# Optimization experiments

Hardware: AMD Instinct MI355X
Metric: run time of the kernel (lower is better)

## Reference

```python
import jax, jax.numpy as jnp
import numpy as np

TOPK = 6
E = 512
IN = 384
M = 8192
LN_EPS = 1e-5


def _lin(x, w, b):
    # torch nn.Linear: y = x @ W^T + b, W is [out, in]
    return x @ w.T + b


def setup_inputs() -> dict:
    key = jax.random.key(0)
    ks = jax.random.split(key, 16)
    s = lambda k, sh: (jax.random.normal(k, sh, dtype=jnp.float32) * 0.02)
    return {
        "x": jax.random.normal(ks[0], (1, M, IN), dtype=jnp.float32),
        "fc1_w": s(ks[1], (E, IN)), "fc1_b": jnp.zeros((E,), jnp.float32),
        "wh_w": s(ks[2], (E, E)),   "wh_b": jnp.zeros((E,), jnp.float32),
        "wt_w": s(ks[3], (E, E)),   "wt_b": jnp.zeros((E,), jnp.float32),
        "l1_w": s(ks[4], (E, E)),   "l1_b": jnp.zeros((E,), jnp.float32),
        "l2_w": s(ks[5], (E, E)),   "l2_b": jnp.zeros((E,), jnp.float32),
        "a1_w": s(ks[6], (E // 2, E)), "a1_b": jnp.zeros((E // 2,), jnp.float32),
        "a2_w": s(ks[7], (1, E // 2)), "a2_b": jnp.zeros((1,), jnp.float32),
        "ln_g": jnp.ones((E,), jnp.float32), "ln_b": jnp.zeros((E,), jnp.float32),
    }


def reference(x, fc1_w, fc1_b, wh_w, wh_b, wt_w, wt_b,
              l1_w, l1_b, l2_w, l2_b, a1_w, a1_b, a2_w, a2_b, ln_g, ln_b):
    lrelu = jax.nn.leaky_relu  # slope 0.01 == torch default
    h = lrelu(_lin(x, fc1_w, fc1_b))                      # [B,M,E]
    h = (h + h.mean(axis=1, keepdims=True)) * 0.5
    e_h = _lin(h, wh_w, wh_b)                             # [B,M,E]
    e_t = _lin(h, wt_w, wt_b)                             # [B,M,E]
    scale = E ** (-0.5)
    attn_logit = (e_h * scale) @ jnp.swapaxes(e_t, -2, -1)  # [B,M,M]
    topk_weight, topk_index = jax.lax.top_k(attn_logit, TOPK)  # [B,M,K]
    # gather top-k neighbor tail embeddings: [B,M,K,E]
    Nb_h = jax.vmap(lambda et, idx: et[idx])(e_t, topk_index)
    topk_prob = jax.nn.softmax(topk_weight, axis=2)       # [B,M,K]
    eh_r = topk_prob[..., None] * Nb_h + (1.0 - topk_prob)[..., None] * e_h[:, :, None, :]
    gate = jnp.tanh(e_h[:, :, None, :] + eh_r)            # [B,M,K,E]
    # faithful to torch einsum('ijkl,ijkm->ijk'): sums l and m independently
    ka_weight = Nb_h.sum(axis=-1) * gate.sum(axis=-1)     # [B,M,K]
    ka_prob = jax.nn.softmax(ka_weight, axis=2)           # [B,M,K]
    e_Nh = jnp.einsum('bmk,bmke->bme', ka_prob, Nb_h)     # [B,M,E]
    sum_emb = lrelu(_lin(e_h + e_Nh, l1_w, l1_b))
    bi_emb = lrelu(_lin(e_h * e_Nh, l2_w, l2_b))
    emb = sum_emb + bi_emb                                # [B,M,E] (dropout = eval identity)
    hn = emb[0]                                           # squeeze(0) -> [M,E]
    # GeoGlobalAttention readout: gate_nn = Linear->LeakyReLU->Linear, softmax over nodes
    g = _lin(lrelu(_lin(hn, a1_w, a1_b)), a2_w, a2_b)     # [M,1]
    att = jax.nn.softmax(g, axis=0)
    pooled = (att * hn).sum(axis=0, keepdims=True)        # [1,E]
    mu = pooled.mean(axis=-1, keepdims=True)
    var = jnp.mean((pooled - mu) ** 2, axis=-1, keepdims=True)
    out = (pooled - mu) / jnp.sqrt(var + LN_EPS) * ln_g + ln_b
    return out
```

## Files before the change

kernel.cpp:

```cpp
#include <hip/hip_runtime.h>
#include <math.h>
#include <stdint.h>

#define M_NODES 8192
#define E_DIM   512
#define NTOPK   6
#define ATTN_SCALE 0.04419417382415922f
#define NEG_BIG (-1e38f)
#define CAND_CAP 192

typedef __attribute__((ext_vector_type(8))) short short8;
typedef __attribute__((ext_vector_type(4))) float f32x4;

__device__ __forceinline__ float lrelu(float v) { return v > 0.f ? v : 0.01f * v; }

__device__ __forceinline__ unsigned short f2bf(float f) {
  uint32_t u = __float_as_uint(f);
  uint32_t r = (u + 0x7FFFu + ((u >> 16) & 1u)) >> 16;
  return (unsigned short)r;
}
__device__ __forceinline__ float bf2f(unsigned short s) {
  return __uint_as_float(((uint32_t)s) << 16);
}

__device__ __forceinline__ void async_cp16(const void* gptr, void* lds) {
  auto g1 = reinterpret_cast<const __attribute__((address_space(1))) unsigned int*>(
      reinterpret_cast<uintptr_t>(gptr));
  auto l3 = reinterpret_cast<__attribute__((address_space(3))) unsigned int*>(
      reinterpret_cast<uintptr_t>(lds));
  __builtin_amdgcn_global_load_lds(g1, l3, 16, 0, 0);
}



__global__ __launch_bounds__(256) void wcast_kernel(
    const float* __restrict__ x, const float* __restrict__ fc1w,
    const float* __restrict__ whw, const float* __restrict__ wtw,
    const float* __restrict__ l1w, const float* __restrict__ l2w,
    const float* __restrict__ a1w,
    unsigned short* __restrict__ xT, unsigned short* __restrict__ fc1T,
    unsigned short* __restrict__ whT, unsigned short* __restrict__ wtT,
    unsigned short* __restrict__ l1T, unsigned short* __restrict__ l2T,
    unsigned short* __restrict__ a1T)
{
  const int gid = blockIdx.x * 256 + threadIdx.x;
  const float* src; unsigned short* dst; int K8, local;
  if (gid < 417792) {
    K8 = 48;
    if (gid < 393216) { src = x; dst = xT; local = gid; }
    else { src = fc1w; dst = fc1T; local = gid - 393216; }
  } else {
    K8 = 64;
    if (gid < 450560)      { src = whw; dst = whT; local = gid - 417792; }
    else if (gid < 483328) { src = wtw; dst = wtT; local = gid - 450560; }
    else if (gid < 516096) { src = l1w; dst = l1T; local = gid - 483328; }
    else if (gid < 548864) { src = l2w; dst = l2T; local = gid - 516096; }
    else                   { src = a1w; dst = a1T; local = gid - 548864; }
  }
  const int m = local / K8;
  const int k8 = local - m * K8;
  const float* p = src + (size_t)m * (K8 * 8) + k8 * 8;
  float4 v0 = ((const float4*)p)[0];
  float4 v1 = ((const float4*)p)[1];
  const int Kt = K8 >> 2;
  const size_t ti = ((size_t)(m >> 4) * Kt + (k8 >> 2)) * 512 + ((m & 15) + 16 * (k8 & 3)) * 8;
  uint4 pk;
  pk.x = (uint32_t)f2bf(v0.x) | ((uint32_t)f2bf(v0.y) << 16);
  pk.y = (uint32_t)f2bf(v0.z) | ((uint32_t)f2bf(v0.w) << 16);
  pk.z = (uint32_t)f2bf(v1.x) | ((uint32_t)f2bf(v1.y) << 16);
  pk.w = (uint32_t)f2bf(v1.z) | ((uint32_t)f2bf(v1.w) << 16);
  *(uint4*)(dst + ti) = pk;
}

template <int MODE>
__global__ __launch_bounds__(256) void mfma_gemm(
    const unsigned short* __restrict__ At1, const unsigned short* __restrict__ At2,
    const unsigned short* __restrict__ Wt1, const unsigned short* __restrict__ Wt2,
    const float* __restrict__ b1, const float* __restrict__ b2,
    float* __restrict__ Cf, unsigned short* __restrict__ T1,
    unsigned short* __restrict__ T2, unsigned short* __restrict__ Cbf,
    unsigned short* __restrict__ Cbf2, int N, int K)
{
  constexpr bool DUALW = (MODE == 1 || MODE == 2);
  __shared__ unsigned short As[2][8 * 512];
  __shared__ unsigned short Bs[2][4 * 512];
  const int Kt = K >> 5;
  const int tid = threadIdx.x, lane = tid & 63, w = tid >> 6;
  const int m0 = blockIdx.y * 128, n0 = blockIdx.x * 64;

  f32x4 acc0[2][4], acc1[2][4];
#pragma unroll
  for (int p = 0; p < 2; p++)
#pragma unroll
    for (int j = 0; j < 4; j++) {
      acc0[p][j] = (f32x4){0.f, 0.f, 0.f, 0.f};
      acc1[p][j] = (f32x4){0.f, 0.f, 0.f, 0.f};
    }

  for (int kt = 0; kt < Kt; kt++) {
    const unsigned short* a1p = At1 + ((size_t)((m0 >> 4) + 2 * w) * Kt + kt) * 512 + lane * 8;
    async_cp16(a1p, &As[0][(2 * w) * 512]);
    async_cp16(a1p + (size_t)Kt * 512, &As[0][(2 * w + 1) * 512]);
    if (MODE == 2) {
      const unsigned short* a2p = At2 + ((size_t)((m0 >> 4) + 2 * w) * Kt + kt) * 512 + lane * 8;
      async_cp16(a2p, &As[1][(2 * w) * 512]);
      async_cp16(a2p + (size_t)Kt * 512, &As[1][(2 * w + 1) * 512]);
    }
    const unsigned short* bp1 = Wt1 + ((size_t)((n0 >> 4) + w) * Kt + kt) * 512 + lane * 8;
    async_cp16(bp1, &Bs[0][w * 512]);
    if (DUALW) {
      const unsigned short* bp2 = Wt2 + ((size_t)((n0 >> 4) + w) * Kt + kt) * 512 + lane * 8;
      async_cp16(bp2, &Bs[1][w * 512]);
    }
    __syncthreads();
    short8 a[2], a2[2], bb[4], bb2[4];
#pragma unroll
    for (int p = 0; p < 2; p++) a[p] = *(const short8*)&As[0][(2 * w + p) * 512 + lane * 8];
    if (MODE == 2) {
#pragma unroll
      for (int p = 0; p < 2; p++) a2[p] = *(const short8*)&As[1][(2 * w + p) * 512 + lane * 8];
    }
#pragma unroll
    for (int j = 0; j < 4; j++) bb[j] = *(const short8*)&Bs[0][j * 512 + lane * 8];
    if (DUALW) {
#pragma unroll
      for (int j = 0; j < 4; j++) bb2[j] = *(const short8*)&Bs[1][j * 512 + lane * 8];
    }
#pragma unroll
    for (int p = 0; p < 2; p++)
#pragma unroll
      for (int j = 0; j < 4; j++) {
        acc0[p][j] = __builtin_amdgcn_mfma_f32_16x16x32_bf16(a[p], bb[j], acc0[p][j], 0, 0, 0);
        if (MODE == 1)
          acc1[p][j] = __builtin_amdgcn_mfma_f32_16x16x32_bf16(a[p], bb2[j], acc1[p][j], 0, 0, 0);
        if (MODE == 2)
          acc1[p][j] = __builtin_amdgcn_mfma_f32_16x16x32_bf16(a2[p], bb2[j], acc1[p][j], 0, 0, 0);
      }
    __syncthreads();
  }

  const int lrow = (lane >> 4) * 4, lcol = lane & 15;

  if (MODE == 3) {
    float part[2][4] = {};
#pragma unroll
    for (int p = 0; p < 2; p++)
#pragma unroll
      for (int j = 0; j < 4; j++) {
        const int c = n0 + j * 16 + lcol;
        const float bias1 = b1[c];
        const float w2 = b2[c];
#pragma unroll
        for (int d = 0; d < 4; d++)
          part[p][d] = fmaf(lrelu(acc0[p][j][d] + bias1), w2, part[p][d]);
      }
#pragma unroll
    for (int p = 0; p < 2; p++)
#pragma unroll
      for (int d = 0; d < 4; d++) {
#pragma unroll
        for (int off = 1; off < 16; off <<= 1)
          part[p][d] += __shfl_xor(part[p][d], off);
      }
    if (lcol == 0) {
#pragma unroll
      for (int p = 0; p < 2; p++)
#pragma unroll
        for (int d = 0; d < 4; d++)
          atomicAdd(&Cf[m0 + w * 32 + p * 16 + lrow + d], part[p][d]);
    }
    return;
  }

  const int NT = N >> 5;
#pragma unroll
  for (int p = 0; p < 2; p++)
#pragma unroll
    for (int j = 0; j < 4; j++) {
      const int c = n0 + j * 16 + lcol;
      const float bias1 = b1[c];
      const float bias2 = DUALW ? b2[c] : 0.f;
#pragma unroll
      for (int d = 0; d < 4; d++) {
        const int r = m0 + w * 32 + p * 16 + lrow + d;
        const float v0 = acc0[p][j][d] + bias1;
        if (MODE == 0) {
          Cf[(size_t)r * N + c] = lrelu(v0);
        } else {
          const size_t ti = ((size_t)(r >> 4) * NT + (c >> 5)) * 512 +
                            ((r & 15) + 16 * ((c >> 3) & 3)) * 8 + (c & 7);
          if (MODE == 1) {
            const float v1 = acc1[p][j][d] + bias2;
            T1[ti] = f2bf(v0);
            T2[ti] = f2bf(v1);
            Cbf[(size_t)r * N + c] = f2bf(v0);
            Cbf2[(size_t)r * N + c] = f2bf(v1);
          } else {
            const float e = lrelu(v0) + lrelu(acc1[p][j][d] + bias2);
            T1[ti] = f2bf(e);
            Cbf[(size_t)r * N + c] = f2bf(e);
          }
        }
      }
    }
}

__global__ __launch_bounds__(256) void colsum_kernel(const float* __restrict__ h,
                                                     float* __restrict__ colsum)
{
  const int t = threadIdx.x;
  const int r0 = blockIdx.x * 128;
  float s0 = 0.f, s1 = 0.f;
  for (int r = 0; r < 128; r++) {
    s0 += h[(size_t)(r0 + r) * E_DIM + t];
    s1 += h[(size_t)(r0 + r) * E_DIM + 256 + t];
  }
  atomicAdd(&colsum[t], s0);
  atomicAdd(&colsum[t + 256], s1);
}

__global__ __launch_bounds__(256) void hupd_cast_kernel(
    const float* __restrict__ h, const float* __restrict__ colsum,
    unsigned short* __restrict__ hT)
{
  const int gid = blockIdx.x * 256 + threadIdx.x;
  const int m = gid >> 6, k8 = gid & 63;
  const float* p = h + (size_t)m * E_DIM + k8 * 8;
  float4 v0 = ((const float4*)p)[0];
  float4 v1 = ((const float4*)p)[1];
  float4 c0 = *(const float4*)(colsum + k8 * 8);
  float4 c1 = *(const float4*)(colsum + k8 * 8 + 4);
  const float im = 1.f / (float)M_NODES;
  v0.x = (v0.x + c0.x * im) * 0.5f; v0.y = (v0.y + c0.y * im) * 0.5f;
  v0.z = (v0.z + c0.z * im) * 0.5f; v0.w = (v0.w + c0.w * im) * 0.5f;
  v1.x = (v1.x + c1.x * im) * 0.5f; v1.y = (v1.y + c1.y * im) * 0.5f;
  v1.z = (v1.z + c1.z * im) * 0.5f; v1.w = (v1.w + c1.w * im) * 0.5f;
  const size_t ti = ((size_t)(m >> 4) * 16 + (k8 >> 2)) * 512 + ((m & 15) + 16 * (k8 & 3)) * 8;
  uint4 pk;
  pk.x = (uint32_t)f2bf(v0.x) | ((uint32_t)f2bf(v0.y) << 16);
  pk.y = (uint32_t)f2bf(v0.z) | ((uint32_t)f2bf(v0.w) << 16);
  pk.z = (uint32_t)f2bf(v1.x) | ((uint32_t)f2bf(v1.y) << 16);
  pk.w = (uint32_t)f2bf(v1.z) | ((uint32_t)f2bf(v1.w) << 16);
  *(uint4*)(hT + ti) = pk;
}

__global__ __launch_bounds__(256, 4) void sgemm_kernel(
    const unsigned short* __restrict__ ehT, const unsigned short* __restrict__ etT,
    unsigned short* __restrict__ sc, float* __restrict__ tmax)
{
  __shared__ unsigned short As[8 * 512];
  __shared__ unsigned short Bs[8 * 512];
  const int tid = threadIdx.x, lane = tid & 63, w = tid >> 6;
  const int wr = w >> 1, wc = w & 1;
  const int m0 = blockIdx.y * 128;
  const int n0 = blockIdx.x * 128;

  f32x4 acc[4][4];
#pragma unroll
  for (int i = 0; i < 4; i++)
#pragma unroll
    for (int j = 0; j < 4; j++) acc[i][j] = (f32x4){0.f, 0.f, 0.f, 0.f};

  for (int kt = 0; kt < 16; kt++) {
    const int s0 = w, s1 = w + 4;
    async_cp16(ehT + ((size_t)((m0 >> 4) + s0) * 16 + kt) * 512 + lane * 8, &As[s0 * 512]);
    async_cp16(ehT + ((size_t)((m0 >> 4) + s1) * 16 + kt) * 512 + lane * 8, &As[s1 * 512]);
    async_cp16(etT + ((size_t)((n0 >> 4) + s0) * 16 + kt) * 512 + lane * 8, &Bs[s0 * 512]);
    async_cp16(etT + ((size_t)((n0 >> 4) + s1) * 16 + kt) * 512 + lane * 8, &Bs[s1 * 512]);
    __syncthreads();
    short8 a[4], b[4];
#pragma unroll
    for (int i = 0; i < 4; i++) a[i] = *(const short8*)&As[(wr * 4 + i) * 512 + lane * 8];
#pragma unroll
    for (int j = 0; j < 4; j++) b[j] = *(const short8*)&Bs[(wc * 4 + j) * 512 + lane * 8];
#pragma unroll
    for (int i = 0; i < 4; i++)
#pragma unroll
      for (int j = 0; j < 4; j++)
        acc[i][j] = __builtin_amdgcn_mfma_f32_16x16x32_bf16(a[i], b[j], acc[i][j], 0, 0, 0);
    __syncthreads();
  }

  const int q = lane >> 4, lcol = lane & 15;
  const size_t blkbase = ((size_t)blockIdx.y * 64 + blockIdx.x) * 16384;

  float rm[4][4];
#pragma unroll
  for (int i = 0; i < 4; i++)
#pragma unroll
    for (int d = 0; d < 4; d++) rm[i][d] = NEG_BIG;

#pragma unroll
  for (int i = 0; i < 4; i++)
#pragma unroll
    for (int jj = 0; jj < 2; jj++) {
      unsigned short o[8];
#pragma unroll
      for (int d = 0; d < 4; d++) {
        o[d] = f2bf(acc[i][2 * jj][d]);
        o[4 + d] = f2bf(acc[i][2 * jj + 1][d]);
        rm[i][d] = fmaxf(rm[i][d], fmaxf(bf2f(o[d]), bf2f(o[4 + d])));
      }
      const size_t off = blkbase + (size_t)(wr * 4 + i) * 2048 + q * 512 +
                         (wc * 32 + jj * 16 + lcol) * 8;
      *(short8*)(sc + off) = *(short8*)o;
    }

#pragma unroll
  for (int i = 0; i < 4; i++)
#pragma unroll
    for (int d = 0; d < 4; d++) {
#pragma unroll
      for (int off = 1; off < 16; off <<= 1)
        rm[i][d] = fmaxf(rm[i][d], __shfl_xor(rm[i][d], off));
    }

  if (lcol == 0) {
#pragma unroll
    for (int i = 0; i < 4; i++)
#pragma unroll
      for (int d = 0; d < 4; d++)
        tmax[(size_t)(m0 + wr * 64 + i * 16 + q * 4 + d) * 128 +
             blockIdx.x * 2 + wc] = rm[i][d];
  }
}

__global__ __launch_bounds__(256) void scan_topk_kernel(
    const unsigned short* __restrict__ sc, const float* __restrict__ tmax,
    float* __restrict__ tkv, int* __restrict__ tki)
{
  __shared__ float cv[4][CAND_CAP];
  __shared__ int   ci[4][CAND_CAP];
  __shared__ int   cnt[4];
  __shared__ float taus[4];
  const int tid = threadIdx.x;
  const int lane = tid & 63;
  const int w = tid >> 6;
  const int rg = blockIdx.x;
  const int bm = rg >> 5;
  const int g = rg & 31;
  const int wr = g >> 4, gi = (g >> 2) & 3, gq = g & 3;
  const int r0 = bm * 128 + wr * 64 + gi * 16 + gq * 4;

  if (tid < 4) cnt[tid] = 0;

  {
    const float* tm = tmax + (size_t)(r0 + w) * 128;
    const float v2 = fmaxf(tm[lane], tm[lane + 64]);
    uint32_t u = __float_as_uint(v2);
    u = ((int)u >= 0) ? (u | 0x80000000u) : ~u;
    uint32_t key = (u & ~63u) | (uint32_t)lane;
    float tau = 0.f;
#pragma unroll
    for (int it = 0; it < 6; it++) {
      uint32_t k = key;
#pragma unroll
      for (int off = 32; off; off >>= 1) {
        const uint32_t o = (uint32_t)__shfl_xor((int)k, off);
        k = k > o ? k : o;
      }
      const int wl = (int)(k & 63u);
      if (it == 5) tau = __shfl(v2, wl);
      if (lane == wl) key = 0u;
    }
    if (lane == 0) taus[w] = tau;
  }
  __syncthreads();
  const float t0 = taus[0], t1 = taus[1], t2 = taus[2], t3 = taus[3];

  const size_t rowoff = (size_t)(wr * 4 + gi) * 2048 + gq * 512 + lane * 8;
  const int colbase = (lane >> 5) * 64 + 2 * ((lane >> 4) & 1) * 16 + (lane & 15);
  for (int t = 0; t < 16; t++) {
    const int bn = w * 16 + t;
    short8 u = *(const short8*)(sc + ((size_t)(bm * 64 + bn)) * 16384 + rowoff);
    const int cb = bn * 128 + colbase;
#pragma unroll
    for (int e = 0; e < 8; e++) {
      const float f = bf2f((unsigned short)u[e]);
      const int d = e & 3;
      const float tau = (d == 0) ? t0 : (d == 1) ? t1 : (d == 2) ? t2 : t3;
      if (f >= tau) {
        const int slot = atomicAdd(&cnt[d], 1);
        if (slot < CAND_CAP) {
          cv[d][slot] = f;
          ci[d][slot] = cb + (e >> 2) * 16;
        }
      }
    }
  }
  __syncthreads();

  int n = cnt[w];
  n = n < CAND_CAP ? n : CAND_CAP;
  for (int c = lane; c < n; c += 64) {
    const float v = cv[w][c];
    const int idx = ci[w][c];
    int rank = 0;
    for (int j = 0; j < n; j++) {
      const float vj = cv[w][j];
      rank += (vj > v) || (vj == v && ci[w][j] < idx);
    }
    if (rank < NTOPK) {
      const size_t base = (size_t)(r0 + w) * NTOPK + rank;
      tkv[base] = v * ATTN_SCALE;
      tki[base] = idx;
    }
  }
}

__global__ __launch_bounds__(256) void combine_kernel(
    const unsigned short* __restrict__ ehRow, const unsigned short* __restrict__ etRow,
    const float* __restrict__ tkv, const int* __restrict__ tki,
    unsigned short* __restrict__ s1T, unsigned short* __restrict__ s2T)
{
  const int lane = threadIdx.x & 63;
  const int m = blockIdx.x * 4 + (threadIdx.x >> 6);

  float wv[NTOPK]; int id[NTOPK];
#pragma unroll
  for (int k = 0; k < NTOPK; k++) {
    wv[k] = tkv[(size_t)m * NTOPK + k];
    id[k] = tki[(size_t)m * NTOPK + k];
  }

  float mx = wv[0];
#pragma unroll
  for (int k = 1; k < NTOPK; k++) mx = fmaxf(mx, wv[k]);
  float p[NTOPK]; float s = 0.f;
#pragma unroll
  for (int k = 0; k < NTOPK; k++) { p[k] = expf(wv[k] - mx); s += p[k]; }
  const float inv = 1.f / s;
#pragma unroll
  for (int k = 0; k < NTOPK; k++) p[k] *= inv;

  short8 eh8 = *(const short8*)(ehRow + (size_t)m * E_DIM + lane * 8);
  float ehv[8];
#pragma unroll
  for (int e = 0; e < 8; e++) ehv[e] = bf2f((unsigned short)eh8[e]);

  float nv[NTOPK][8];
#pragma unroll
  for (int k = 0; k < NTOPK; k++) {
    short8 nb = *(const short8*)(etRow + (size_t)id[k] * E_DIM + lane * 8);
#pragma unroll
    for (int e = 0; e < 8; e++) nv[k][e] = bf2f((unsigned short)nb[e]);
  }

  float ka[NTOPK];
#pragma unroll
  for (int k = 0; k < NTOPK; k++) {
    float snb = 0.f, sg = 0.f;
    const float aa = 2.f - p[k], bb = p[k];
#pragma unroll
    for (int e = 0; e < 8; e++) {
      snb += nv[k][e];
      sg += tanhf(fmaf(aa, ehv[e], bb * nv[k][e]));
    }
#pragma unroll
    for (int off = 32; off; off >>= 1) {
      snb += __shfl_xor(snb, off);
      sg += __shfl_xor(sg, off);
    }
    ka[k] = snb * sg;
  }
  float km = ka[0];
#pragma unroll
  for (int k = 1; k < NTOPK; k++) km = fmaxf(km, ka[k]);
  float kp[NTOPK]; float ks = 0.f;
#pragma unroll
  for (int k = 0; k < NTOPK; k++) { kp[k] = expf(ka[k] - km); ks += kp[k]; }
  const float kinv = 1.f / ks;

  const size_t tbase = ((size_t)(m >> 4) * 16 + (lane >> 2)) * 512 +
                       ((m & 15) + 16 * (lane & 3)) * 8;
  unsigned short o1[8], o2[8];
#pragma unroll
  for (int e = 0; e < 8; e++) {
    float o = 0.f;
#pragma unroll
    for (int k = 0; k < NTOPK; k++) o = fmaf(kp[k], nv[k][e], o);
    o *= kinv;
    o1[e] = f2bf(ehv[e] + o);
    o2[e] = f2bf(ehv[e] * o);
  }
  *(short8*)(s1T + tbase) = *(short8*)o1;
  *(short8*)(s2T + tbase) = *(short8*)o2;
}

__global__ __launch_bounds__(1024) void softmax_stats_kernel(
    const float* __restrict__ g, float* __restrict__ stats)
{
  __shared__ float red[16];
  __shared__ float red2[16];
  const int t = threadIdx.x;
  float mx = NEG_BIG;
  for (int i = t; i < M_NODES; i += 1024) mx = fmaxf(mx, g[i]);
#pragma unroll
  for (int off = 32; off; off >>= 1) mx = fmaxf(mx, __shfl_xor(mx, off));
  if ((t & 63) == 0) red[t >> 6] = mx;
  __syncthreads();
  float gmx = red[0];
  for (int i = 1; i < 16; i++) gmx = fmaxf(gmx, red[i]);
  float s = 0.f;
  for (int i = t; i < M_NODES; i += 1024) s += expf(g[i] - gmx);
#pragma unroll
  for (int off = 32; off; off >>= 1) s += __shfl_xor(s, off);
  if ((t & 63) == 0) red2[t >> 6] = s;
  __syncthreads();
  if (t == 0) {
    float tot = 0.f;
    for (int i = 0; i < 16; i++) tot += red2[i];
    stats[0] = gmx; stats[1] = tot;
  }
}

__global__ __launch_bounds__(256) void pooled_kernel(
    const unsigned short* __restrict__ emb, const float* __restrict__ g,
    const float* __restrict__ stats, float* __restrict__ pooled)
{
  const int t = threadIdx.x;
  const int r0 = blockIdx.x * 128;
  const float mx = stats[0];
  const float inv = 1.f / stats[1];
  float a0 = 0.f, a1 = 0.f;
  for (int r = 0; r < 128; r++) {
    const int m = r0 + r;
    const float wv = expf(g[m] - mx) * inv;
    a0 = fmaf(wv, bf2f(emb[(size_t)m * E_DIM + t]), a0);
    a1 = fmaf(wv, bf2f(emb[(size_t)m * E_DIM + 256 + t]), a1);
  }
  atomicAdd(&pooled[t], a0);
  atomicAdd(&pooled[t + 256], a1);
}

__global__ __launch_bounds__(512) void ln_kernel(
    const float* __restrict__ pooled, const float* __restrict__ lng,
    const float* __restrict__ lnb, float* __restrict__ out)
{
  __shared__ float red[8];
  __shared__ float red2[8];
  const int t = threadIdx.x;
  const float v = pooled[t];
  float s = v;
#pragma unroll
  for (int off = 32; off; off >>= 1) s += __shfl_xor(s, off);
  if ((t & 63) == 0) red[t >> 6] = s;
  __syncthreads();
  float tot = 0.f;
  for (int i = 0; i < 8; i++) tot += red[i];
  const float mu = tot / (float)E_DIM;
  const float d = v - mu;
  float q = d * d;
#pragma unroll
  for (int off = 32; off; off >>= 1) q += __shfl_xor(q, off);
  if ((t & 63) == 0) red2[t >> 6] = q;
  __syncthreads();
  float vt = 0.f;
  for (int i = 0; i < 8; i++) vt += red2[i];
  const float var = vt / (float)E_DIM;
  out[t] = d * rsqrtf(var + 1e-5f) * lng[t] + lnb[t];
}

extern "C" void kernel_launch(void* const* d_in, const int* in_sizes, int n_in,
                              void* d_out, int out_size, void* d_ws, size_t ws_size,
                              hipStream_t stream)
{
  const float* x     = (const float*)d_in[0];
  const float* fc1_w = (const float*)d_in[1];
  const float* fc1_b = (const float*)d_in[2];
  const float* wh_w  = (const float*)d_in[3];
  const float* wh_b  = (const float*)d_in[4];
  const float* wt_w  = (const float*)d_in[5];
  const float* wt_b  = (const float*)d_in[6];
  const float* l1_w  = (const float*)d_in[7];
  const float* l1_b  = (const float*)d_in[8];
  const float* l2_w  = (const float*)d_in[9];
  const float* l2_b  = (const float*)d_in[10];
  const float* a1_w  = (const float*)d_in[11];
  const float* a1_b  = (const float*)d_in[12];
  const float* a2_w  = (const float*)d_in[13];
  const float* a2_b  = (const float*)d_in[14];
  const float* ln_g  = (const float*)d_in[15];
  const float* ln_b  = (const float*)d_in[16];
  (void)a2_b;

  char* ws = (char*)d_ws;
  const size_t MiB = 1 << 20;
  unsigned short* fc1T = (unsigned short*)(ws + 0);
  unsigned short* whT  = (unsigned short*)(ws + 393216);
  unsigned short* wtT  = (unsigned short*)(ws + 917504);
  unsigned short* l1T  = (unsigned short*)(ws + 1441792);
  unsigned short* l2T  = (unsigned short*)(ws + 1966080);
  unsigned short* a1T  = (unsigned short*)(ws + 2490368);
  unsigned short* xT     = (unsigned short*)(ws + 3 * MiB);
  float*          h      = (float*)(ws + 9 * MiB);
  unsigned short* hT     = (unsigned short*)(ws + 25 * MiB);
  unsigned short* ehT    = (unsigned short*)(ws + 33 * MiB);
  unsigned short* etT    = (unsigned short*)(ws + 41 * MiB);
  unsigned short* ehRow  = (unsigned short*)(ws + 49 * MiB);
  unsigned short* etRow  = (unsigned short*)(ws + 57 * MiB);
  float*          tmaxb  = (float*)(ws + 65 * MiB);
  unsigned short* s1T    = (unsigned short*)(ws + 3 * MiB);
  unsigned short* s2T    = (unsigned short*)(ws + 11 * MiB);
  unsigned short* embT   = (unsigned short*)(ws + 19 * MiB);
  unsigned short* embRow = (unsigned short*)(ws + 27 * MiB);
  unsigned short* scores = (unsigned short*)(ws + 96 * MiB);
  char*           smal   = ws + 69 * MiB;
  float* tkv    = (float*)(smal);
  int*   tki    = (int*)(smal + 196608);
  float* colsum = (float*)(smal + 393216);
  float* g      = (float*)(smal + 395264);
  float* stats  = (float*)(smal + 428032);
  float* pooled = (float*)(smal + 432128);

  hipMemsetAsync(smal, 0, 436224, stream);

  wcast_kernel<<<2208, 256, 0, stream>>>(x, fc1_w, wh_w, wt_w, l1_w, l2_w, a1_w,
                                         xT, fc1T, whT, wtT, l1T, l2T, a1T);
  mfma_gemm<0><<<dim3(8, 64), 256, 0, stream>>>(
      xT, nullptr, fc1T, nullptr, fc1_b, nullptr, h, nullptr, nullptr, nullptr, nullptr,
      512, 384);
  colsum_kernel<<<64, 256, 0, stream>>>(h, colsum);
  hupd_cast_kernel<<<2048, 256, 0, stream>>>(h, colsum, hT);
  mfma_gemm<1><<<dim3(8, 64), 256, 0, stream>>>(
      hT, nullptr, whT, wtT, wh_b, wt_b, nullptr, ehT, etT, ehRow, etRow, 512, 512);
  sgemm_kernel<<<dim3(64, 64), 256, 0, stream>>>(ehT, etT, scores, tmaxb);
  scan_topk_kernel<<<M_NODES / 4, 256, 0, stream>>>(scores, tmaxb, tkv, tki);
  combine_kernel<<<M_NODES / 4, 256, 0, stream>>>(ehRow, etRow, tkv, tki, s1T, s2T);
  mfma_gemm<2><<<dim3(8, 64), 256, 0, stream>>>(
      s1T, s2T, l1T, l2T, l1_b, l2_b, nullptr, embT, nullptr, embRow, nullptr, 512, 512);
  mfma_gemm<3><<<dim3(4, 64), 256, 0, stream>>>(
      embT, nullptr, a1T, nullptr, a1_b, a2_w, g, nullptr, nullptr, nullptr, nullptr,
      256, 512);
  softmax_stats_kernel<<<1, 1024, 0, stream>>>(g, stats);
  pooled_kernel<<<64, 256, 0, stream>>>(embRow, g, stats, pooled);
  ln_kernel<<<1, 512, 0, stream>>>(pooled, ln_g, ln_b, (float*)d_out);
}
```

Before: 323.0 us.

## Fuse colsum into fc1 GEMM, merge top-k scan with combine, drop softmax stats

The fc1 GEMM now writes bf16 rows and accumulates column sums with atomics, which removes the separate fp32 h buffer and the colsum pass. The score matrix is stored row-major per 128-column block, and the scan uses per-block maxima to skip blocks that cannot hold a top-6 candidate. The scan is fused with the combine kernel so top-k results stay in shared memory. The softmax-statistics kernel is dropped in favour of unnormalised exp weights plus an atomic sum that ln divides out. This risks overflow without max subtraction, and rounding h to bf16 before the mean changes precision.

```diff
diff --git a/kernel.cpp b/kernel.cpp
--- a/kernel.cpp
+++ b/kernel.cpp
@@ -172,6 +172,35 @@
     return;
   }
 
+  if (MODE == 4) {
+    float colp[4] = {};
+#pragma unroll
+    for (int p = 0; p < 2; p++)
+#pragma unroll
+      for (int j = 0; j < 4; j++) {
+        const int c = n0 + j * 16 + lcol;
+        const float bias1 = b1[c];
+#pragma unroll
+        for (int d = 0; d < 4; d++) {
+          const int r = m0 + w * 32 + p * 16 + lrow + d;
+          const float v = lrelu(acc0[p][j][d] + bias1);
+          Cbf[(size_t)r * N + c] = f2bf(v);
+          colp[j] += v;
+        }
+      }
+#pragma unroll
+    for (int j = 0; j < 4; j++) {
+      colp[j] += __shfl_xor(colp[j], 16);
+      colp[j] += __shfl_xor(colp[j], 32);
+    }
+    if (lane < 16) {
+#pragma unroll
+      for (int j = 0; j < 4; j++)
+        atomicAdd(&Cf[n0 + j * 16 + lcol], colp[j]);
+    }
+    return;
+  }
+
   const int NT = N >> 5;
 #pragma unroll
   for (int p = 0; p < 2; p++)
@@ -184,63 +213,46 @@
       for (int d = 0; d < 4; d++) {
         const int r = m0 + w * 32 + p * 16 + lrow + d;
         const float v0 = acc0[p][j][d] + bias1;
-        if (MODE == 0) {
-          Cf[(size_t)r * N + c] = lrelu(v0);
+        const size_t ti = ((size_t)(r >> 4) * NT + (c >> 5)) * 512 +
+                          ((r & 15) + 16 * ((c >> 3) & 3)) * 8 + (c & 7);
+        if (MODE == 1) {
+          const float v1 = acc1[p][j][d] + bias2;
+          T1[ti] = f2bf(v0);
+          T2[ti] = f2bf(v1);
+          Cbf[(size_t)r * N + c] = f2bf(v0);
+          Cbf2[(size_t)r * N + c] = f2bf(v1);
         } else {
-          const size_t ti = ((size_t)(r >> 4) * NT + (c >> 5)) * 512 +
-                            ((r & 15) + 16 * ((c >> 3) & 3)) * 8 + (c & 7);
-          if (MODE == 1) {
-            const float v1 = acc1[p][j][d] + bias2;
-            T1[ti] = f2bf(v0);
-            T2[ti] = f2bf(v1);
-            Cbf[(size_t)r * N + c] = f2bf(v0);
-            Cbf2[(size_t)r * N + c] = f2bf(v1);
-          } else {
-            const float e = lrelu(v0) + lrelu(acc1[p][j][d] + bias2);
-            T1[ti] = f2bf(e);
-            Cbf[(size_t)r * N + c] = f2bf(e);
-          }
+          const float e = lrelu(v0) + lrelu(acc1[p][j][d] + bias2);
+          T1[ti] = f2bf(e);
+          Cbf[(size_t)r * N + c] = f2bf(e);
         }
       }
     }
 }
 
-__global__ __launch_bounds__(256) void colsum_kernel(const float* __restrict__ h,
-                                                     float* __restrict__ colsum)
-{
-  const int t = threadIdx.x;
-  const int r0 = blockIdx.x * 128;
-  float s0 = 0.f, s1 = 0.f;
-  for (int r = 0; r < 128; r++) {
-    s0 += h[(size_t)(r0 + r) * E_DIM + t];
-    s1 += h[(size_t)(r0 + r) * E_DIM + 256 + t];
-  }
-  atomicAdd(&colsum[t], s0);
-  atomicAdd(&colsum[t + 256], s1);
-}
-
 __global__ __launch_bounds__(256) void hupd_cast_kernel(
-    const float* __restrict__ h, const float* __restrict__ colsum,
+    const unsigned short* __restrict__ hRow, const float* __restrict__ colsum,
     unsigned short* __restrict__ hT)
 {
   const int gid = blockIdx.x * 256 + threadIdx.x;
   const int m = gid >> 6, k8 = gid & 63;
-  const float* p = h + (size_t)m * E_DIM + k8 * 8;
-  float4 v0 = ((const float4*)p)[0];
-  float4 v1 = ((const float4*)p)[1];
+  short8 hv = *(const short8*)(hRow + (size_t)m * E_DIM + k8 * 8);
   float4 c0 = *(const float4*)(colsum + k8 * 8);
   float4 c1 = *(const float4*)(colsum + k8 * 8 + 4);
   const float im = 1.f / (float)M_NODES;
-  v0.x = (v0.x + c0.x * im) * 0.5f; v0.y = (v0.y + c0.y * im) * 0.5f;
-  v0.z = (v0.z + c0.z * im) * 0.5f; v0.w = (v0.w + c0.w * im) * 0.5f;
-  v1.x = (v1.x + c1.x * im) * 0.5f; v1.y = (v1.y + c1.y * im) * 0.5f;
-  v1.z = (v1.z + c1.z * im) * 0.5f; v1.w = (v1.w + c1.w * im) * 0.5f;
+  float v[8];
+#pragma unroll
+  for (int e = 0; e < 8; e++) v[e] = bf2f((unsigned short)hv[e]);
+  v[0] = (v[0] + c0.x * im) * 0.5f; v[1] = (v[1] + c0.y * im) * 0.5f;
+  v[2] = (v[2] + c0.z * im) * 0.5f; v[3] = (v[3] + c0.w * im) * 0.5f;
+  v[4] = (v[4] + c1.x * im) * 0.5f; v[5] = (v[5] + c1.y * im) * 0.5f;
+  v[6] = (v[6] + c1.z * im) * 0.5f; v[7] = (v[7] + c1.w * im) * 0.5f;
   const size_t ti = ((size_t)(m >> 4) * 16 + (k8 >> 2)) * 512 + ((m & 15) + 16 * (k8 & 3)) * 8;
   uint4 pk;
-  pk.x = (uint32_t)f2bf(v0.x) | ((uint32_t)f2bf(v0.y) << 16);
-  pk.y = (uint32_t)f2bf(v0.z) | ((uint32_t)f2bf(v0.w) << 16);
-  pk.z = (uint32_t)f2bf(v1.x) | ((uint32_t)f2bf(v1.y) << 16);
-  pk.w = (uint32_t)f2bf(v1.z) | ((uint32_t)f2bf(v1.w) << 16);
+  pk.x = (uint32_t)f2bf(v[0]) | ((uint32_t)f2bf(v[1]) << 16);
+  pk.y = (uint32_t)f2bf(v[2]) | ((uint32_t)f2bf(v[3]) << 16);
+  pk.z = (uint32_t)f2bf(v[4]) | ((uint32_t)f2bf(v[5]) << 16);
+  pk.w = (uint32_t)f2bf(v[6]) | ((uint32_t)f2bf(v[7]) << 16);
   *(uint4*)(hT + ti) = pk;
 }
 
@@ -282,7 +294,7 @@
   }
 
   const int q = lane >> 4, lcol = lane & 15;
-  const size_t blkbase = ((size_t)blockIdx.y * 64 + blockIdx.x) * 16384;
+  const int bn = blockIdx.x;
 
   float rm[4][4];
 #pragma unroll
@@ -293,17 +305,16 @@
 #pragma unroll
   for (int i = 0; i < 4; i++)
 #pragma unroll
-    for (int jj = 0; jj < 2; jj++) {
-      unsigned short o[8];
-#pragma unroll
-      for (int d = 0; d < 4; d++) {
-        o[d] = f2bf(acc[i][2 * jj][d]);
-        o[4 + d] = f2bf(acc[i][2 * jj + 1][d]);
-        rm[i][d] = fmaxf(rm[i][d], fmaxf(bf2f(o[d]), bf2f(o[4 + d])));
+    for (int d = 0; d < 4; d++) {
+      unsigned short o[4];
+#pragma unroll
+      for (int j = 0; j < 4; j++) {
+        o[j] = f2bf(acc[i][j][d]);
+        rm[i][d] = fmaxf(rm[i][d], bf2f(o[j]));
       }
-      const size_t off = blkbase + (size_t)(wr * 4 + i) * 2048 + q * 512 +
-                         (wc * 32 + jj * 16 + lcol) * 8;
-      *(short8*)(sc + off) = *(short8*)o;
+      const int row = m0 + wr * 64 + i * 16 + q * 4 + d;
+      const size_t off = ((size_t)row * 64 + bn) * 128 + (wc * 16 + lcol) * 4;
+      *(uint2*)(sc + off) = *(uint2*)o;
     }
 
 #pragma unroll
@@ -321,70 +332,65 @@
 #pragma unroll
       for (int d = 0; d < 4; d++)
         tmax[(size_t)(m0 + wr * 64 + i * 16 + q * 4 + d) * 128 +
-             blockIdx.x * 2 + wc] = rm[i][d];
-  }
-}
-
-__global__ __launch_bounds__(256) void scan_topk_kernel(
+             bn * 2 + wc] = rm[i][d];
+  }
+}
+
+__global__ __launch_bounds__(256) void scan_combine_kernel(
     const unsigned short* __restrict__ sc, const float* __restrict__ tmax,
-    float* __restrict__ tkv, int* __restrict__ tki)
+    const unsigned short* __restrict__ ehRow, const unsigned short* __restrict__ etRow,
+    unsigned short* __restrict__ s1T, unsigned short* __restrict__ s2T)
 {
   __shared__ float cv[4][CAND_CAP];
   __shared__ int   ci[4][CAND_CAP];
   __shared__ int   cnt[4];
-  __shared__ float taus[4];
+  __shared__ float t6v[4][8];
+  __shared__ int   t6i[4][8];
   const int tid = threadIdx.x;
   const int lane = tid & 63;
   const int w = tid >> 6;
-  const int rg = blockIdx.x;
-  const int bm = rg >> 5;
-  const int g = rg & 31;
-  const int wr = g >> 4, gi = (g >> 2) & 3, gq = g & 3;
-  const int r0 = bm * 128 + wr * 64 + gi * 16 + gq * 4;
-
-  if (tid < 4) cnt[tid] = 0;
-
-  {
-    const float* tm = tmax + (size_t)(r0 + w) * 128;
-    const float v2 = fmaxf(tm[lane], tm[lane + 64]);
-    uint32_t u = __float_as_uint(v2);
-    u = ((int)u >= 0) ? (u | 0x80000000u) : ~u;
-    uint32_t key = (u & ~63u) | (uint32_t)lane;
-    float tau = 0.f;
-#pragma unroll
-    for (int it = 0; it < 6; it++) {
-      uint32_t k = key;
-#pragma unroll
-      for (int off = 32; off; off >>= 1) {
-        const uint32_t o = (uint32_t)__shfl_xor((int)k, off);
-        k = k > o ? k : o;
-      }
-      const int wl = (int)(k & 63u);
-      if (it == 5) tau = __shfl(v2, wl);
-      if (lane == wl) key = 0u;
-    }
-    if (lane == 0) taus[w] = tau;
-  }
-  __syncthreads();
-  const float t0 = taus[0], t1 = taus[1], t2 = taus[2], t3 = taus[3];
-
-  const size_t rowoff = (size_t)(wr * 4 + gi) * 2048 + gq * 512 + lane * 8;
-  const int colbase = (lane >> 5) * 64 + 2 * ((lane >> 4) & 1) * 16 + (lane & 15);
-  for (int t = 0; t < 16; t++) {
-    const int bn = w * 16 + t;
-    short8 u = *(const short8*)(sc + ((size_t)(bm * 64 + bn)) * 16384 + rowoff);
-    const int cb = bn * 128 + colbase;
-#pragma unroll
-    for (int e = 0; e < 8; e++) {
-      const float f = bf2f((unsigned short)u[e]);
-      const int d = e & 3;
-      const float tau = (d == 0) ? t0 : (d == 1) ? t1 : (d == 2) ? t2 : t3;
+  const int row = blockIdx.x * 4 + w;
+
+  if (lane == 0) cnt[w] = 0;
+  if (lane < 8) { t6v[w][lane] = 0.f; t6i[w][lane] = 0; }
+
+  const float* tm = tmax + (size_t)row * 128;
+  const float v2 = fmaxf(tm[lane], tm[lane + 64]);
+  const float bmax = fmaxf(tm[2 * lane], tm[2 * lane + 1]);
+  uint32_t u = __float_as_uint(v2);
+  u = ((int)u >= 0) ? (u | 0x80000000u) : ~u;
+  uint32_t key = (u & ~63u) | (uint32_t)lane;
+  float tau = 0.f;
+#pragma unroll
+  for (int it = 0; it < 6; it++) {
+    uint32_t k = key;
+#pragma unroll
+    for (int off = 32; off; off >>= 1) {
+      const uint32_t o = (uint32_t)__shfl_xor((int)k, off);
+      k = k > o ? k : o;
+    }
+    const int wl = (int)(k & 63u);
+    if (it == 5) tau = __shfl(v2, wl);
+    if (lane == wl) key = 0u;
+  }
+
+  unsigned long long mask = __ballot(bmax >= tau);
+  const unsigned short* rp = sc + (size_t)row * 8192;
+  while (mask) {
+    const int bn = __ffsll(mask) - 1;
+    mask &= mask - 1;
+    const uint32_t uu = *(const uint32_t*)(rp + bn * 128 + lane * 2);
+    const float f0 = bf2f((unsigned short)(uu & 0xFFFFu));
+    const float f1 = bf2f((unsigned short)(uu >> 16));
+#pragma unroll
+    for (int e = 0; e < 2; e++) {
+      const float f = e ? f1 : f0;
       if (f >= tau) {
-        const int slot = atomicAdd(&cnt[d], 1);
-        if (slot < CAND_CAP) {
-          cv[d][slot] = f;
-          ci[d][slot] = cb + (e >> 2) * 16;
-        }
+        const int idx128 = lane * 2 + e;
+        const int g = idx128 >> 2, j = idx128 & 3;
+        const int col = bn * 128 + (g >> 4) * 64 + j * 16 + (g & 15);
+        const int slot = atomicAdd(&cnt[w], 1);
+        if (slot < CAND_CAP) { cv[w][slot] = f; ci[w][slot] = col; }
       }
     }
   }
@@ -400,27 +406,16 @@
       const float vj = cv[w][j];
       rank += (vj > v) || (vj == v && ci[w][j] < idx);
     }
-    if (rank < NTOPK) {
-      const size_t base = (size_t)(r0 + w) * NTOPK + rank;
-      tkv[base] = v * ATTN_SCALE;
-      tki[base] = idx;
-    }
-  }
-}
-
-__global__ __launch_bounds__(256) void combine_kernel(
-    const unsigned short* __restrict__ ehRow, const unsigned short* __restrict__ etRow,
-    const float* __restrict__ tkv, const int* __restrict__ tki,
-    unsigned short* __restrict__ s1T, unsigned short* __restrict__ s2T)
-{
-  const int lane = threadIdx.x & 63;
-  const int m = blockIdx.x * 4 + (threadIdx.x >> 6);
-
+    if (rank < NTOPK) { t6v[w][rank] = v; t6i[w][rank] = idx; }
+  }
+  __syncthreads();
+
+  const int m = row;
   float wv[NTOPK]; int id[NTOPK];
 #pragma unroll
   for (int k = 0; k < NTOPK; k++) {
-    wv[k] = tkv[(size_t)m * NTOPK + k];
-    id[k] = tki[(size_t)m * NTOPK + k];
+    wv[k] = t6v[w][k] * ATTN_SCALE;
+    id[k] = t6i[w][k];
   }
 
   float mx = wv[0];
@@ -487,60 +482,34 @@
   *(short8*)(s2T + tbase) = *(short8*)o2;
 }
 
-__global__ __launch_bounds__(1024) void softmax_stats_kernel(
-    const float* __restrict__ g, float* __restrict__ stats)
-{
-  __shared__ float red[16];
-  __shared__ float red2[16];
-  const int t = threadIdx.x;
-  float mx = NEG_BIG;
-  for (int i = t; i < M_NODES; i += 1024) mx = fmaxf(mx, g[i]);
-#pragma unroll
-  for (int off = 32; off; off >>= 1) mx = fmaxf(mx, __shfl_xor(mx, off));
-  if ((t & 63) == 0) red[t >> 6] = mx;
-  __syncthreads();
-  float gmx = red[0];
-  for (int i = 1; i < 16; i++) gmx = fmaxf(gmx, red[i]);
-  float s = 0.f;
-  for (int i = t; i < M_NODES; i += 1024) s += expf(g[i] - gmx);
-#pragma unroll
-  for (int off = 32; off; off >>= 1) s += __shfl_xor(s, off);
-  if ((t & 63) == 0) red2[t >> 6] = s;
-  __syncthreads();
-  if (t == 0) {
-    float tot = 0.f;
-    for (int i = 0; i < 16; i++) tot += red2[i];
-    stats[0] = gmx; stats[1] = tot;
-  }
-}
-
 __global__ __launch_bounds__(256) void pooled_kernel(
     const unsigned short* __restrict__ emb, const float* __restrict__ g,
-    const float* __restrict__ stats, float* __restrict__ pooled)
+    float* __restrict__ pooled, float* __restrict__ wsum)
 {
   const int t = threadIdx.x;
   const int r0 = blockIdx.x * 128;
-  const float mx = stats[0];
-  const float inv = 1.f / stats[1];
-  float a0 = 0.f, a1 = 0.f;
+  float a0 = 0.f, a1 = 0.f, lsum = 0.f;
   for (int r = 0; r < 128; r++) {
     const int m = r0 + r;
-    const float wv = expf(g[m] - mx) * inv;
+    const float wv = expf(g[m]);
+    lsum += wv;
     a0 = fmaf(wv, bf2f(emb[(size_t)m * E_DIM + t]), a0);
     a1 = fmaf(wv, bf2f(emb[(size_t)m * E_DIM + 256 + t]), a1);
   }
   atomicAdd(&pooled[t], a0);
   atomicAdd(&pooled[t + 256], a1);
+  if (t == 0) atomicAdd(wsum, lsum);
 }
 
 __global__ __launch_bounds__(512) void ln_kernel(
-    const float* __restrict__ pooled, const float* __restrict__ lng,
-    const float* __restrict__ lnb, float* __restrict__ out)
+    const float* __restrict__ pooled, const float* __restrict__ wsum,
+    const float* __restrict__ lng, const float* __restrict__ lnb,
+    float* __restrict__ out)
 {
   __shared__ float red[8];
   __shared__ float red2[8];
   const int t = threadIdx.x;
-  const float v = pooled[t];
+  const float v = pooled[t] / wsum[0];
   float s = v;
 #pragma unroll
   for (int off = 32; off; off >>= 1) s += __shfl_xor(s, off);
@@ -593,7 +562,7 @@
   unsigned short* l2T  = (unsigned short*)(ws + 1966080);
   unsigned short* a1T  = (unsigned short*)(ws + 2490368);
   unsigned short* xT     = (unsigned short*)(ws + 3 * MiB);
-  float*          h      = (float*)(ws + 9 * MiB);
+  unsigned short* hRow   = (unsigned short*)(ws + 9 * MiB);
   unsigned short* hT     = (unsigned short*)(ws + 25 * MiB);
   unsigned short* ehT    = (unsigned short*)(ws + 33 * MiB);
   unsigned short* etT    = (unsigned short*)(ws + 41 * MiB);
@@ -606,33 +575,29 @@
   unsigned short* embRow = (unsigned short*)(ws + 27 * MiB);
   unsigned short* scores = (unsigned short*)(ws + 96 * MiB);
   char*           smal   = ws + 69 * MiB;
-  float* tkv    = (float*)(smal);
-  int*   tki    = (int*)(smal + 196608);
-  float* colsum = (float*)(smal + 393216);
-  float* g      = (float*)(smal + 395264);
-  float* stats  = (float*)(smal + 428032);
-  float* pooled = (float*)(smal + 432128);
-
-  hipMemsetAsync(smal, 0, 436224, stream);
+  float* colsum = (float*)(smal);
+  float* g      = (float*)(smal + 4096);
+  float* stats  = (float*)(smal + 36864);
+  float* pooled = (float*)(smal + 40960);
+
+  hipMemsetAsync(smal, 0, 43008, stream);
 
   wcast_kernel<<<2208, 256, 0, stream>>>(x, fc1_w, wh_w, wt_w, l1_w, l2_w, a1_w,
                                          xT, fc1T, whT, wtT, l1T, l2T, a1T);
-  mfma_gemm<0><<<dim3(8, 64), 256, 0, stream>>>(
-      xT, nullptr, fc1T, nullptr, fc1_b, nullptr, h, nullptr, nullptr, nullptr, nullptr,
+  mfma_gemm<4><<<dim3(8, 64), 256, 0, stream>>>(
+      xT, nullptr, fc1T, nullptr, fc1_b, nullptr, colsum, nullptr, nullptr, hRow, nullptr,
       512, 384);
-  colsum_kernel<<<64, 256, 0, stream>>>(h, colsum);
-  hupd_cast_kernel<<<2048, 256, 0, stream>>>(h, colsum, hT);
+  hupd_cast_kernel<<<2048, 256, 0, stream>>>(hRow, colsum, hT);
   mfma_gemm<1><<<dim3(8, 64), 256, 0, stream>>>(
       hT, nullptr, whT, wtT, wh_b, wt_b, nullptr, ehT, etT, ehRow, etRow, 512, 512);
   sgemm_kernel<<<dim3(64, 64), 256, 0, stream>>>(ehT, etT, scores, tmaxb);
-  scan_topk_kernel<<<M_NODES / 4, 256, 0, stream>>>(scores, tmaxb, tkv, tki);
-  combine_kernel<<<M_NODES / 4, 256, 0, stream>>>(ehRow, etRow, tkv, tki, s1T, s2T);
+  scan_combine_kernel<<<M_NODES / 4, 256, 0, stream>>>(
+      scores, tmaxb, ehRow, etRow, s1T, s2T);
   mfma_gemm<2><<<dim3(8, 64), 256, 0, stream>>>(
       s1T, s2T, l1T, l2T, l1_b, l2_b, nullptr, embT, nullptr, embRow, nullptr, 512, 512);
   mfma_gemm<3><<<dim3(4, 64), 256, 0, stream>>>(
       embT, nullptr, a1T, nullptr, a1_b, a2_w, g, nullptr, nullptr, nullptr, nullptr,
       256, 512);
-  softmax_stats_kernel<<<1, 1024, 0, stream>>>(g, stats);
-  pooled_kernel<<<64, 256, 0, stream>>>(embRow, g, stats, pooled);
-  ln_kernel<<<1, 512, 0, stream>>>(pooled, ln_g, ln_b, (float*)d_out);
-}
+  pooled_kernel<<<64, 256, 0, stream>>>(embRow, g, pooled, stats);
+  ln_kernel<<<1, 512, 0, stream>>>(pooled, stats, ln_g, ln_b, (float*)d_out);
+}
```

Result: faster. 306.3 us (-5.1%).
